# Kernel tuning notes

Measured on AMD Instinct MI355X. Metric: run time of the kernel, lower is better.

Reference implementation:

```python
import jax, jax.numpy as jnp
import numpy as np

N = 100000      # nodes (PF candidates)
E = 1600000     # edges, avg degree 16
CONT = 6        # continuous features
H = 32          # hidden_dim
PDGS = [1, 2, 11, 13, 22, 130, 211]


def _p(k, shape):
    return jax.random.normal(k, shape, jnp.float32) * 0.1


def setup_inputs() -> dict:
    key = jax.random.key(0)
    ks = jax.random.split(key, 24)
    x_cont = jax.random.normal(ks[0], (N, CONT), jnp.float32)
    pdg = jnp.array(PDGS, jnp.int32)[jax.random.randint(ks[1], (N,), 0, 7)]
    sign = jax.random.randint(ks[2], (N,), 0, 2) * 2 - 1
    charge = jax.random.randint(ks[3], (N,), -1, 2)
    pv = jax.random.randint(ks[4], (N,), 0, 8)
    x_cat = jnp.stack([pdg * sign, charge, pv], axis=1).astype(jnp.int32)
    edge_index = jax.random.randint(ks[5], (2, E), 0, N, jnp.int32)
    batch = jnp.zeros((N,), jnp.int32)
    return {
        "x_cont": x_cont, "x_cat": x_cat, "edge_index": edge_index, "batch": batch,
        "W_cont": _p(ks[6], (CONT, H // 2)), "b_cont": jnp.zeros((H // 2,), jnp.float32),
        "T_chrg": _p(ks[7], (3, H // 4)), "T_pdg": _p(ks[8], (7, H // 4)), "T_pv": _p(ks[9], (8, H // 4)),
        "W_cat": _p(ks[10], (3 * H // 4, H // 2)), "b_cat": jnp.zeros((H // 2,), jnp.float32),
        "W_enc": _p(ks[11], (H, H)), "b_enc": jnp.zeros((H,), jnp.float32),
        "g_all": jnp.ones((H,), jnp.float32), "be_all": jnp.zeros((H,), jnp.float32),
        "W_msg": _p(ks[12], (2 * H, H)), "b_msg": jnp.zeros((H,), jnp.float32),
        "g_conv": jnp.ones((H,), jnp.float32), "be_conv": jnp.zeros((H,), jnp.float32),
        "W_out1": _p(ks[13], (H, H // 2)), "b_out1": jnp.zeros((H // 2,), jnp.float32),
        "W_out2": _p(ks[14], (H // 2, 1)), "b_out2": jnp.zeros((1,), jnp.float32),
    }


def _batchnorm(x, gamma, beta, eps=1e-5):
    # training-mode BatchNorm1d: biased batch stats over the node axis
    mu = jnp.mean(x, axis=0)
    var = jnp.mean(jnp.square(x - mu), axis=0)
    return (x - mu) * jax.lax.rsqrt(var + eps) * gamma + beta


def reference(x_cont, x_cat, edge_index, batch,
              W_cont, b_cont, T_chrg, T_pdg, T_pv, W_cat, b_cat,
              W_enc, b_enc, g_all, be_all, W_msg, b_msg, g_conv, be_conv,
              W_out1, b_out1, W_out2, b_out2):
    elu = jax.nn.elu
    emb_cont = elu(x_cont @ W_cont + b_cont)                      # [N, H/2]
    emb_chrg = T_chrg[x_cat[:, 1] + 1]                            # [N, H/4]
    emb_pv = T_pv[x_cat[:, 2]]                                    # [N, H/4]
    pdg_remap = jnp.abs(x_cat[:, 0])
    for i, pdgval in enumerate(PDGS):  # fixed small constant loop, as in original
        pdg_remap = jnp.where(pdg_remap == pdgval, jnp.int32(i), pdg_remap)
    emb_pdg = T_pdg[pdg_remap]                                    # [N, H/4]
    emb_cat = elu(jnp.concatenate([emb_chrg, emb_pdg, emb_pv], axis=1) @ W_cat + b_cat)
    emb = elu(jnp.concatenate([emb_cat, emb_cont], axis=1) @ W_enc + b_enc)
    emb = _batchnorm(emb, g_all, be_all)                          # [N, H]
    # EdgeConv: m_ij = nn([x_i, x_j - x_i]), aggregate by max over incoming edges
    src, dst = edge_index[0], edge_index[1]
    x_i = emb[dst]
    x_j = emb[src]
    msg = jnp.concatenate([x_i, x_j - x_i], axis=1) @ W_msg + b_msg   # [E, H]
    agg = jax.ops.segment_max(msg, dst, num_segments=N)
    agg = jnp.where(jnp.isfinite(agg), agg, 0.0)                  # nodes w/o in-edges -> 0
    emb = emb + _batchnorm(agg, g_conv, be_conv)
    out = elu(emb @ W_out1 + b_out1) @ W_out2 + b_out2            # [N, 1]
    return out.squeeze(-1)
```

## Files before the change

kernel.cpp:

```cpp
#include <hip/hip_runtime.h>
#include <hip/hip_bf16.h>

#define NN 100000
#define EE 1600000
#define NB_SCAN 391

#define NBUCK 782
#define CPAD  16
#define NPART 391
#define NE4   400000
#define CAP   4096
#define CAPSH 12
#define BCAP  2560

typedef __hip_bfloat16 bf16_t;
typedef int int4v __attribute__((ext_vector_type(4)));
typedef float f4 __attribute__((ext_vector_type(4)));

#define PARB  600000
#define EMB   604480
#define PBUF  3804480
#define QBUF  7004480
#define ABUF  10204480
#define SOFF  13404480
#define PART2 (SOFF + 256)
#define CURS  (PART2 + 4096)
#define ROWP2 (CURS + 12512)
#define OFLB  (ROWP2 + 200000)
#define PEB   (OFLB + 3200004)
#define SRCB  (PEB + 3203072)

#define O_WCONT 0
#define O_BCONT 96
#define O_TCHRG 112
#define O_TPDG  136
#define O_TPV   192
#define O_WCAT  256
#define O_BCAT  640
#define O_WENC  656
#define O_BENC  1680
#define O_GALL  1712
#define O_BEALL 1744
#define O_WMSG  1776
#define O_BMSG  3824
#define O_GCONV 3856
#define O_BECONV 3888
#define O_WOUT1 3920
#define O_BOUT1 4432
#define O_WOUT2 4448
#define O_BOUT2 4464
#define NPAR    4465

__device__ __forceinline__ float bf(unsigned short u) {
    return __uint_as_float(((unsigned)u) << 16);
}
__device__ __forceinline__ f4 elu4(f4 v) {
    f4 r;
    r.x = v.x > 0.0f ? v.x : expm1f(v.x);
    r.y = v.y > 0.0f ? v.y : expm1f(v.y);
    r.z = v.z > 0.0f ? v.z : expm1f(v.z);
    r.w = v.w > 0.0f ? v.w : expm1f(v.w);
    return r;
}
__device__ __forceinline__ f4 f4max(f4 a, f4 b) {
    f4 r;
    r.x = fmaxf(a.x, b.x); r.y = fmaxf(a.y, b.y);
    r.z = fmaxf(a.z, b.z); r.w = fmaxf(a.w, b.w);
    return r;
}

struct InitArgs {
    const void* p[19];
    const unsigned short* wdet;
    int*        flagw;
    float*      par;
    int*        curs;
    float*      stats;
    float*      part;
    int*        ofl;
    int*        tcur;
};

__global__ __launch_bounds__(256) void k_init(InitArgs a)
{
    const int offs[20] = {O_WCONT,O_BCONT,O_TCHRG,O_TPDG,O_TPV,O_WCAT,O_BCAT,O_WENC,
                          O_BENC,O_GALL,O_BEALL,O_WMSG,O_BMSG,O_GCONV,O_BECONV,
                          O_WOUT1,O_BOUT1,O_WOUT2,O_BOUT2,NPAR};
    __shared__ int sflag;
    int b = blockIdx.x, tid = threadIdx.x;
    int g = b * 256 + tid;
    if (g < NBUCK) a.curs[g * CPAD] = g << CAPSH;
    if (g < 4096) a.part[g] = 0.0f;
    if (g < 128) a.stats[g] = 0.0f;
    if (g == 0) { a.ofl[0] = 0; *a.tcur = NBUCK << CAPSH; }
    if (b == 0) {
        if (tid == 0) sflag = 0;
        __syncthreads();
        int bad = 0;
        for (int i = tid; i < 1024; i += 256) {
            unsigned e = (a.wdet[i] >> 7) & 0xFFu;
            if (e >= 137u) bad = 1;
        }
        if (bad) atomicOr(&sflag, 1);
        __syncthreads();
        int f32 = sflag;
        if (tid == 0) *a.flagw = f32;
        for (int i = tid; i < NPAR; i += 256) {
            int t = 0;
            while (offs[t + 1] <= i) t++;
            int l = i - offs[t];
            const void* s = a.p[t];
            a.par[i] = f32 ? ((const float*)s)[l] : bf(((const unsigned short*)s)[l]);
        }
    }
}

struct SMemPart {
    int cnt[NBUCK];
    int lstart[NBUCK];
    int gstart[NBUCK];
    int tsum[256];
    unsigned short bkof[4096];
    int staged[4096];
};
struct SMemEmb  { float wc[96], bc[16], tc[24], tp[56], tv[64],
                  wcat[384], bcat[16], we[1024], be[32], ls[64]; };
union SMemA { SMemPart p; SMemEmb e; };

__global__ __launch_bounds__(256, 1) void k_fA(
    const int* __restrict__ eidx, int* __restrict__ curs,
    int* __restrict__ pe, int* __restrict__ ofl, int2* __restrict__ ofl2,
    const void* __restrict__ xc, const int* __restrict__ x_cat,
    const float* __restrict__ par, const int* __restrict__ flag,
    float* __restrict__ emb, float* __restrict__ stats)
{
    __shared__ alignas(16) SMemA sm;
    int tid = threadIdx.x;
    int b = blockIdx.x;

    if (b < NPART) {
        for (int i = tid; i < NBUCK; i += 256) sm.p.cnt[i] = 0;
        __syncthreads();
        const int4v* src4 = (const int4v*)eidx;
        const int4v* dst4 = (const int4v*)(eidx + EE);
        int i0 = b << 10;
        int i1 = i0 + 1024; if (i1 > NE4) i1 = NE4;
        int nE = (i1 - i0) * 4;
        for (int i = i0 + tid; i < i1; i += 256) {
            int4v d = dst4[i];
            atomicAdd(&sm.p.cnt[d.x >> 7], 1);
            atomicAdd(&sm.p.cnt[d.y >> 7], 1);
            atomicAdd(&sm.p.cnt[d.z >> 7], 1);
            atomicAdd(&sm.p.cnt[d.w >> 7], 1);
        }
        __syncthreads();
        int base = tid * 4;
        int c0 = (base     < NBUCK) ? sm.p.cnt[base    ] : 0;
        int c1 = (base + 1 < NBUCK) ? sm.p.cnt[base + 1] : 0;
        int c2 = (base + 2 < NBUCK) ? sm.p.cnt[base + 2] : 0;
        int c3 = (base + 3 < NBUCK) ? sm.p.cnt[base + 3] : 0;
        int s = c0 + c1 + c2 + c3;
        sm.p.tsum[tid] = s;
        __syncthreads();
        for (int off = 1; off < 256; off <<= 1) {
            int x = (tid >= off) ? sm.p.tsum[tid - off] : 0;
            __syncthreads();
            sm.p.tsum[tid] += x;
            __syncthreads();
        }
        int run = sm.p.tsum[tid] - s;
        if (base < NBUCK) {
            sm.p.lstart[base] = run;
            if (c0) sm.p.gstart[base] = atomicAdd(&curs[base * CPAD], c0);
            run += c0;
        }
        if (base + 1 < NBUCK) {
            sm.p.lstart[base + 1] = run;
            if (c1) sm.p.gstart[base + 1] = atomicAdd(&curs[(base + 1) * CPAD], c1);
            run += c1;
        }
        if (base + 2 < NBUCK) {
            sm.p.lstart[base + 2] = run;
            if (c2) sm.p.gstart[base + 2] = atomicAdd(&curs[(base + 2) * CPAD], c2);
            run += c2;
        }
        if (base + 3 < NBUCK) {
            sm.p.lstart[base + 3] = run;
            if (c3) sm.p.gstart[base + 3] = atomicAdd(&curs[(base + 3) * CPAD], c3);
            run += c3;
        }
        __syncthreads();
        for (int i = tid; i < NBUCK; i += 256) {
            int st = sm.p.lstart[i], c = sm.p.cnt[i];
            for (int j = 0; j < c; j++) sm.p.bkof[st + j] = (unsigned short)i;
        }
        __syncthreads();
        for (int i = tid; i < NBUCK; i += 256) sm.p.cnt[i] = 0;
        __syncthreads();
        for (int i = i0 + tid; i < i1; i += 256) {
            int4v s4 = src4[i];
            int4v d4 = dst4[i];
            #define PLACE(SS, DD) { \
                int bk = (DD) >> 7; \
                int r = atomicAdd(&sm.p.cnt[bk], 1); \
                sm.p.staged[sm.p.lstart[bk] + r] = ((SS) << 7) | ((DD) & 127); }
            PLACE(s4.x, d4.x) PLACE(s4.y, d4.y) PLACE(s4.z, d4.z) PLACE(s4.w, d4.w)
            #undef PLACE
        }
        __syncthreads();
        for (int j = tid; j < nE; j += 256) {
            int bk = sm.p.bkof[j];
            int slot = sm.p.gstart[bk] + (j - sm.p.lstart[bk]);
            int packed = sm.p.staged[j];
            if (slot < ((bk + 1) << CAPSH)) pe[slot] = packed;
            else { int oi = atomicAdd(ofl, 1); ofl2[oi] = make_int2(bk, packed); }
        }
        return;
    }

    {
        float* s;
        s=sm.e.wc;   for(int i=tid;i<96;  i+=256) s[i]=par[O_WCONT+i];
        s=sm.e.bc;   for(int i=tid;i<16;  i+=256) s[i]=par[O_BCONT+i];
        s=sm.e.tc;   for(int i=tid;i<24;  i+=256) s[i]=par[O_TCHRG+i];
        s=sm.e.tp;   for(int i=tid;i<56;  i+=256) s[i]=par[O_TPDG+i];
        s=sm.e.tv;   for(int i=tid;i<64;  i+=256) s[i]=par[O_TPV+i];
        s=sm.e.wcat; for(int i=tid;i<384; i+=256) s[i]=par[O_WCAT+i];
        s=sm.e.bcat; for(int i=tid;i<16;  i+=256) s[i]=par[O_BCAT+i];
        s=sm.e.we;   for(int i=tid;i<1024;i+=256) s[i]=par[O_WENC+i];
        s=sm.e.be;   for(int i=tid;i<32;  i+=256) s[i]=par[O_BENC+i];
        if (tid < 64) sm.e.ls[tid] = 0.0f;
    }
    __syncthreads();

    int n = (b - NPART) * 256 + tid;
    float v[64];
    #pragma unroll
    for (int i = 0; i < 64; i++) v[i] = 0.0f;

    if (n < NN) {
        f4* sWc4 = (f4*)sm.e.wc;  f4* sbc4 = (f4*)sm.e.bc;
        f4* sTc4 = (f4*)sm.e.tc;  f4* sTp4 = (f4*)sm.e.tp;  f4* sTv4 = (f4*)sm.e.tv;
        f4* sWcat4 = (f4*)sm.e.wcat; f4* sbcat4 = (f4*)sm.e.bcat;
        f4* sWe4 = (f4*)sm.e.we;  f4* sbe4 = (f4*)sm.e.be;

        float x0,x1,x2,x3,x4,x5;
        if (*flag) {
            const float* xr = (const float*)xc + (size_t)n * 6;
            x0=xr[0]; x1=xr[1]; x2=xr[2]; x3=xr[3]; x4=xr[4]; x5=xr[5];
        } else {
            const unsigned* xr = (const unsigned*)xc + (size_t)n * 3;
            unsigned w0=xr[0], w1=xr[1], w2=xr[2];
            x0=__uint_as_float(w0<<16); x1=__uint_as_float(w0 & 0xFFFF0000u);
            x2=__uint_as_float(w1<<16); x3=__uint_as_float(w1 & 0xFFFF0000u);
            x4=__uint_as_float(w2<<16); x5=__uint_as_float(w2 & 0xFFFF0000u);
        }

        f4 ec[4];
        #pragma unroll
        for (int g = 0; g < 4; g++) {
            f4 acc = sbc4[g];
            acc += x0 * sWc4[0*4+g]; acc += x1 * sWc4[1*4+g]; acc += x2 * sWc4[2*4+g];
            acc += x3 * sWc4[3*4+g]; acc += x4 * sWc4[4*4+g]; acc += x5 * sWc4[5*4+g];
            ec[g] = elu4(acc);
        }

        int c0 = x_cat[n*3+0], c1 = x_cat[n*3+1], c2 = x_cat[n*3+2];
        int a0 = c0 < 0 ? -c0 : c0;
        int pi = (a0==1)?0:(a0==2)?1:(a0==11)?2:(a0==13)?3:(a0==22)?4:(a0==130)?5:6;
        int ci = c1 + 1;

        f4 t0a = sTc4[ci*2],  t0b = sTc4[ci*2+1];
        f4 t1a = sTp4[pi*2],  t1b = sTp4[pi*2+1];
        f4 t2a = sTv4[c2*2],  t2b = sTv4[c2*2+1];

        f4 ecat[4];
        #pragma unroll
        for (int g = 0; g < 4; g++) {
            f4 acc = sbcat4[g];
            #pragma unroll
            for (int k = 0; k < 4; k++) acc += t0a[k] * sWcat4[(k     )*4+g];
            #pragma unroll
            for (int k = 0; k < 4; k++) acc += t0b[k] * sWcat4[(4 + k )*4+g];
            #pragma unroll
            for (int k = 0; k < 4; k++) acc += t1a[k] * sWcat4[(8 + k )*4+g];
            #pragma unroll
            for (int k = 0; k < 4; k++) acc += t1b[k] * sWcat4[(12 + k)*4+g];
            #pragma unroll
            for (int k = 0; k < 4; k++) acc += t2a[k] * sWcat4[(16 + k)*4+g];
            #pragma unroll
            for (int k = 0; k < 4; k++) acc += t2b[k] * sWcat4[(20 + k)*4+g];
            ecat[g] = elu4(acc);
        }

        f4* o = (f4*)(emb + (size_t)n * 32);
        #pragma unroll
        for (int cg = 0; cg < 8; cg++) {
            f4 acc = sbe4[cg];
            #pragma unroll
            for (int kg = 0; kg < 4; kg++) {
                #pragma unroll
                for (int k = 0; k < 4; k++)
                    acc += ecat[kg][k] * sWe4[(kg*4+k)*8 + cg];
            }
            #pragma unroll
            for (int kg = 0; kg < 4; kg++) {
                #pragma unroll
                for (int k = 0; k < 4; k++)
                    acc += ec[kg][k] * sWe4[(16 + kg*4+k)*8 + cg];
            }
            f4 val = elu4(acc);
            o[cg] = val;
            #pragma unroll
            for (int k = 0; k < 4; k++) {
                v[cg*4+k]      = val[k];
                v[32+cg*4+k]   = val[k] * val[k];
            }
        }
    }

    int lane = tid & 63;
    #pragma unroll
    for (int st = 0; st < 6; st++) {
        int off = 1 << st;
        int keep = (lane >> st) & 1;
        int L2 = 32 >> st;
        #pragma unroll
        for (int i = 0; i < 32; i++) {
            if (i < L2) {
                float lo = v[i], hi = v[L2 + i];
                float sent = keep ? lo : hi;
                float got = __shfl_xor(sent, off);
                v[i] = (keep ? hi : lo) + got;
            }
        }
    }
    int idx = ((lane&1)<<5)|((lane&2)<<3)|((lane&4)<<1)|((lane&8)>>1)|((lane&16)>>3)|((lane&32)>>5);
    atomicAdd(&sm.e.ls[idx], v[0]);
    __syncthreads();
    if (tid < 64) atomicAdd(&stats[tid], sm.e.ls[tid]);
}

struct SMemCsr { int stage[BCAP]; int cnt[128]; int sc[128]; int ex[128]; int tl; };
struct SMemPq  { float wp[1024], wq[1024], bp[32], bq[32], ssc[32], ssh[32]; };
union SMemB { SMemCsr c; SMemPq q; };

__global__ __launch_bounds__(256) void k_fB(
    const int* __restrict__ curs, const int* __restrict__ pe,
    const int* __restrict__ ofl, const int2* __restrict__ ofl2,
    int* __restrict__ tcur, int2* __restrict__ rowp2, int* __restrict__ srcl,
    const float* __restrict__ emb, const float* __restrict__ stats,
    const float* __restrict__ par, float* __restrict__ P, float* __restrict__ Q)
{
    __shared__ alignas(16) SMemB sm;
    int tid = threadIdx.x;
    int b = blockIdx.x;

    if (b < NBUCK) {
        int beg = b << CAPSH;
        int m_res = curs[b * CPAD] - beg;
        int stored = m_res < CAP ? m_res : CAP;
        int no = ofl[0];
        if (tid < 128) sm.c.cnt[tid] = 0;
        __syncthreads();
        for (int i = tid; i < stored; i += 256) {
            int p = pe[beg + i];
            if (i < BCAP) sm.c.stage[i] = p;
            atomicAdd(&sm.c.cnt[p & 127], 1);
        }
        for (int j = tid; j < no; j += 256) {
            int2 oe = ofl2[j];
            if (oe.x == b) atomicAdd(&sm.c.cnt[oe.y & 127], 1);
        }
        __syncthreads();
        if (tid < 128) sm.c.sc[tid] = sm.c.cnt[tid];
        __syncthreads();
        for (int off = 1; off < 128; off <<= 1) {
            int x = (tid >= off && tid < 128) ? sm.c.sc[tid - off] : 0;
            __syncthreads();
            if (tid < 128) sm.c.sc[tid] += x;
            __syncthreads();
        }
        int obeg = beg;
        if (m_res > CAP) {
            if (tid == 0) sm.c.tl = atomicAdd(tcur, m_res);
            __syncthreads();
            obeg = sm.c.tl;
        }
        if (tid < 128) {
            int e0 = sm.c.sc[tid] - sm.c.cnt[tid];
            int deg = sm.c.cnt[tid];
            sm.c.ex[tid] = e0;
            int node = b * 128 + tid;
            if (node < NN) rowp2[node] = make_int2(obeg + e0, obeg + e0 + deg);
            sm.c.cnt[tid] = 0;
        }
        __syncthreads();
        for (int i = tid; i < stored; i += 256) {
            int p = (i < BCAP) ? sm.c.stage[i] : pe[beg + i];
            int dl = p & 127;
            int r = atomicAdd(&sm.c.cnt[dl], 1);
            srcl[obeg + sm.c.ex[dl] + r] = p >> 7;
        }
        for (int j = tid; j < no; j += 256) {
            int2 oe = ofl2[j];
            if (oe.x == b) {
                int dl = oe.y & 127;
                int r = atomicAdd(&sm.c.cnt[dl], 1);
                srcl[obeg + sm.c.ex[dl] + r] = oe.y >> 7;
            }
        }
        return;
    }

    if (tid < 32) {
        float mu  = stats[tid] * (1.0f / NN);
        float var = stats[32 + tid] * (1.0f / NN) - mu * mu;
        float s   = par[O_GALL + tid] * rsqrtf(var + 1e-5f);
        sm.q.ssc[tid] = s;
        sm.q.ssh[tid] = par[O_BEALL + tid] - mu * s;
    }
    __syncthreads();
    for (int e = tid; e < 1024; e += 256) {
        int k = e >> 5;
        float w1 = par[O_WMSG + e];
        float w2 = par[O_WMSG + 1024 + e];
        sm.q.wp[e] = sm.q.ssc[k] * (w1 - w2);
        sm.q.wq[e] = sm.q.ssc[k] * w2;
    }
    if (tid < 32) {
        float aP = par[O_BMSG + tid], aQ = 0.0f;
        for (int k = 0; k < 32; k++) {
            float w1 = par[O_WMSG + k*32 + tid];
            float w2 = par[O_WMSG + (k+32)*32 + tid];
            aP += sm.q.ssh[k] * (w1 - w2);
            aQ += sm.q.ssh[k] * w2;
        }
        sm.q.bp[tid] = aP;
        sm.q.bq[tid] = aQ;
    }
    __syncthreads();

    int n = (b - NBUCK) * 256 + tid;
    if (n >= NN) return;

    f4* sWP4 = (f4*)sm.q.wp; f4* sWQ4 = (f4*)sm.q.wq;
    f4* sbP4 = (f4*)sm.q.bp; f4* sbQ4 = (f4*)sm.q.bq;
    const f4* er = (const f4*)(emb + (size_t)n * 32);
    f4 e[8];
    #pragma unroll
    for (int g = 0; g < 8; g++) e[g] = er[g];
    f4* pr = (f4*)(P + (size_t)n * 32);
    f4* qr = (f4*)(Q + (size_t)n * 32);
    #pragma unroll
    for (int cg = 0; cg < 8; cg++) {
        f4 aP = sbP4[cg];
        f4 aQ = sbQ4[cg];
        #pragma unroll
        for (int kg = 0; kg < 8; kg++) {
            #pragma unroll
            for (int k = 0; k < 4; k++) {
                float ek = e[kg][k];
                aP += ek * sWP4[(kg*4+k)*8 + cg];
                aQ += ek * sWQ4[(kg*4+k)*8 + cg];
            }
        }
        pr[cg] = aP;
        qr[cg] = aQ;
    }
}

__global__ __launch_bounds__(256) void k_gather(
    const int2* __restrict__ rowp2, const int* __restrict__ srcl,
    const float* __restrict__ Q, const float* __restrict__ P,
    float* __restrict__ agg, float* __restrict__ part)
{
    __shared__ float ls[64];
    int tid = threadIdx.x;
    if (tid < 64) ls[tid] = 0.0f;
    __syncthreads();

    int lane = tid & 63;
    int wave = tid >> 6;
    int n = blockIdx.x * 4 + wave;
    int slice = lane >> 3;
    int cg    = lane & 7;
    int2 be = rowp2[n];
    int beg = be.x, end = be.y;
    const f4* Q4 = (const f4*)Q;

    f4 pv = (f4){0.f, 0.f, 0.f, 0.f};
    if (lane < 8 && end > beg) pv = ((const f4*)P)[(size_t)n * 8 + lane];

    f4 m = {-INFINITY, -INFINITY, -INFINITY, -INFINITY};
    for (int e = beg + slice; e < end; e += 32) {
        int e1 = min(e + 8,  end - 1);
        int e2 = min(e + 16, end - 1);
        int e3 = min(e + 24, end - 1);
        int s0 = __builtin_nontemporal_load(&srcl[e]);
        int s1 = __builtin_nontemporal_load(&srcl[e1]);
        int s2 = __builtin_nontemporal_load(&srcl[e2]);
        int s3 = __builtin_nontemporal_load(&srcl[e3]);
        f4 q0 = Q4[(size_t)s0 * 8 + cg];
        f4 q1 = Q4[(size_t)s1 * 8 + cg];
        f4 q2 = Q4[(size_t)s2 * 8 + cg];
        f4 q3 = Q4[(size_t)s3 * 8 + cg];
        q0 = f4max(q0, q1);
        q2 = f4max(q2, q3);
        m = f4max(m, f4max(q0, q2));
    }
    #pragma unroll
    for (int off = 8; off < 64; off <<= 1) {
        m.x = fmaxf(m.x, __shfl_xor(m.x, off));
        m.y = fmaxf(m.y, __shfl_xor(m.y, off));
        m.z = fmaxf(m.z, __shfl_xor(m.z, off));
        m.w = fmaxf(m.w, __shfl_xor(m.w, off));
    }
    if (lane < 8) {
        f4 o;
        if (end > beg) o = m + pv;
        else           o = (f4){0.f, 0.f, 0.f, 0.f};
        ((f4*)agg)[(size_t)n * 8 + lane] = o;
        atomicAdd(&ls[cg*4+0], o.x);
        atomicAdd(&ls[cg*4+1], o.y);
        atomicAdd(&ls[cg*4+2], o.z);
        atomicAdd(&ls[cg*4+3], o.w);
        atomicAdd(&ls[32+cg*4+0], o.x*o.x);
        atomicAdd(&ls[32+cg*4+1], o.y*o.y);
        atomicAdd(&ls[32+cg*4+2], o.z*o.z);
        atomicAdd(&ls[32+cg*4+3], o.w*o.w);
    }
    __syncthreads();
    if (tid < 64) atomicAdd(&part[(blockIdx.x & 63) * 64 + tid], ls[tid]);
}

__global__ __launch_bounds__(256, 1) void k_out(
    const float* __restrict__ emb, const float* __restrict__ agg,
    const float* __restrict__ par, const float* __restrict__ stats,
    const float* __restrict__ part,
    const int* __restrict__ flag, void* __restrict__ out)
{
    __shared__ f4 sW14[128];
    __shared__ f4 sb14[4], sW24[4];
    __shared__ f4 sc14[8], sh14[8], sc24[8], sh24[8];
    __shared__ float spart[64];
    __shared__ float sb2s;
    int tid = threadIdx.x;
    {
        float* s = (float*)sW14;
        for (int i = tid; i < 512; i += 256) s[i] = par[O_WOUT1 + i];
    }
    if (tid < 16) {
        ((float*)sb14)[tid] = par[O_BOUT1 + tid];
        ((float*)sW24)[tid] = par[O_WOUT2 + tid];
    }
    if (tid < 64) {
        float acc2 = 0.0f;
        #pragma unroll 8
        for (int r = 0; r < 64; r++) acc2 += part[r * 64 + tid];
        spart[tid] = acc2;
    }
    if (tid == 0) sb2s = par[O_BOUT2];
    __syncthreads();
    if (tid < 32) {
        float mu  = stats[tid] * (1.0f / NN);
        float var = stats[32 + tid] * (1.0f / NN) - mu * mu;
        float s   = par[O_GALL + tid] * rsqrtf(var + 1e-5f);
        ((float*)sc14)[tid] = s;
        ((float*)sh14)[tid] = par[O_BEALL + tid] - mu * s;
        float mu2  = spart[tid] * (1.0f / NN);
        float var2 = spart[32 + tid] * (1.0f / NN) - mu2 * mu2;
        float s2   = par[O_GCONV + tid] * rsqrtf(var2 + 1e-5f);
        ((float*)sc24)[tid] = s2;
        ((float*)sh24)[tid] = par[O_BECONV + tid] - mu2 * s2;
    }
    __syncthreads();

    int n = blockIdx.x * 256 + tid;
    if (n >= NN) return;

    const f4* er = (const f4*)(emb + (size_t)n * 32);
    const f4* ar = (const f4*)(agg + (size_t)n * 32);
    f4 h[8];
    #pragma unroll
    for (int g = 0; g < 8; g++) {
        f4 ev = er[g];
        f4 av = ar[g];
        h[g] = ev * sc14[g] + sh14[g] + av * sc24[g] + sh24[g];
    }
    f4 o1[4];
    #pragma unroll
    for (int g = 0; g < 4; g++) {
        f4 acc = sb14[g];
        #pragma unroll
        for (int kg = 0; kg < 8; kg++) {
            #pragma unroll
            for (int k = 0; k < 4; k++)
                acc += h[kg][k] * sW14[(kg*4+k)*4 + g];
        }
        o1[g] = elu4(acc);
    }
    float acc = sb2s;
    #pragma unroll
    for (int g = 0; g < 4; g++) {
        f4 p = o1[g] * sW24[g];
        acc += p.x + p.y + p.z + p.w;
    }

    if (*flag) ((float*)out)[n] = acc;
    else       ((bf16_t*)out)[n] = __float2bfloat16(acc);
}


extern "C" void kernel_launch(void* const* d_in, const int* in_sizes, int n_in,
                              void* d_out, int out_size, void* d_ws, size_t ws_size,
                              hipStream_t stream)
{
    const void* x_cont = d_in[0];
    const int* x_cat = (const int*)d_in[1];
    const int* eidx  = (const int*)d_in[2];

    float* ws    = (float*)d_ws;
    float* par   = ws + PARB;
    float* emb   = ws + EMB;
    float* P     = ws + PBUF;
    float* Q     = ws + QBUF;
    float* agg   = ws + ABUF;
    float* stats = ws + SOFF;
    int*   flag  = (int*)(stats + 128);
    int*   tcur  = (int*)(stats + 130);
    float* part  = ws + PART2;
    int*   curs  = (int*)(ws + CURS);
    int2*  rowp2 = (int2*)(ws + ROWP2);
    int*   ofl   = (int*)(ws + OFLB);
    int2*  ofl2  = (int2*)(ws + OFLB + 2);
    int*   pe    = (int*)(ws + PEB);
    int*   srcl  = (int*)(ws + SRCB);

    InitArgs ia;
    for (int t = 0; t < 19; t++) ia.p[t] = d_in[4 + t];
    ia.wdet = (const unsigned short*)d_in[11];
    ia.flagw = flag; ia.par = par; ia.curs = curs; ia.stats = stats;
    ia.part = part; ia.ofl = ofl; ia.tcur = tcur;
    k_init<<<16, 256, 0, stream>>>(ia);

    k_fA<<<NPART + NB_SCAN, 256, 0, stream>>>(eidx, curs, pe, ofl, ofl2,
                                              x_cont, x_cat, par, flag, emb, stats);
    k_fB<<<NBUCK + NB_SCAN, 256, 0, stream>>>(curs, pe, ofl, ofl2, tcur, rowp2, srcl,
                                              emb, stats, par, P, Q);
    k_gather<<<NN / 4, 256, 0, stream>>>(rowp2, srcl, Q, P, agg, part);
    k_out<<<NB_SCAN, 256, 0, stream>>>(emb, agg, par, stats, part, flag, d_out);
}
```

Before: 265.6 us.

## Use half-wave per node in gather and move BN stats to separate kernel

k_gather now handles two nodes per wavefront, 32 lanes each. Each iteration covers 16 edges instead of 32, which suits the average in-degree of 16 and keeps fewer lanes idle. The per-block LDS atomic reduction of BatchNorm sums is taken out of the gather and done by a new grid-stride k_stats kernel that writes into stats[64..127]. k_out reads those sums directly instead of summing the 64-row partial buffer. The cost is an extra kernel launch and a second full read of the agg buffer.

```diff
diff --git a/kernel.cpp b/kernel.cpp
--- a/kernel.cpp
+++ b/kernel.cpp
@@ -23,8 +23,7 @@
 #define QBUF  7004480
 #define ABUF  10204480
 #define SOFF  13404480
-#define PART2 (SOFF + 256)
-#define CURS  (PART2 + 4096)
+#define CURS  (SOFF + 256)
 #define ROWP2 (CURS + 12512)
 #define OFLB  (ROWP2 + 200000)
 #define PEB   (OFLB + 3200004)
@@ -76,7 +75,6 @@
     float*      par;
     int*        curs;
     float*      stats;
-    float*      part;
     int*        ofl;
     int*        tcur;
 };
@@ -90,7 +88,6 @@
     int b = blockIdx.x, tid = threadIdx.x;
     int g = b * 256 + tid;
     if (g < NBUCK) a.curs[g * CPAD] = g << CAPSH;
-    if (g < 4096) a.part[g] = 0.0f;
     if (g < 128) a.stats[g] = 0.0f;
     if (g == 0) { a.ofl[0] = 0; *a.tcur = NBUCK << CAPSH; }
     if (b == 0) {
@@ -473,30 +470,28 @@
 __global__ __launch_bounds__(256) void k_gather(
     const int2* __restrict__ rowp2, const int* __restrict__ srcl,
     const float* __restrict__ Q, const float* __restrict__ P,
-    float* __restrict__ agg, float* __restrict__ part)
+    float* __restrict__ agg)
 {
-    __shared__ float ls[64];
     int tid = threadIdx.x;
-    if (tid < 64) ls[tid] = 0.0f;
-    __syncthreads();
-
     int lane = tid & 63;
     int wave = tid >> 6;
-    int n = blockIdx.x * 4 + wave;
-    int slice = lane >> 3;
-    int cg    = lane & 7;
+    int half  = lane >> 5;
+    int hl    = lane & 31;
+    int slice = hl >> 3;
+    int cg    = hl & 7;
+    int n = (blockIdx.x * 4 + wave) * 2 + half;
     int2 be = rowp2[n];
     int beg = be.x, end = be.y;
     const f4* Q4 = (const f4*)Q;
 
     f4 pv = (f4){0.f, 0.f, 0.f, 0.f};
-    if (lane < 8 && end > beg) pv = ((const f4*)P)[(size_t)n * 8 + lane];
+    if (hl < 8 && end > beg) pv = ((const f4*)P)[(size_t)n * 8 + hl];
 
     f4 m = {-INFINITY, -INFINITY, -INFINITY, -INFINITY};
-    for (int e = beg + slice; e < end; e += 32) {
-        int e1 = min(e + 8,  end - 1);
-        int e2 = min(e + 16, end - 1);
-        int e3 = min(e + 24, end - 1);
+    for (int e = beg + slice; e < end; e += 16) {
+        int e1 = min(e + 4,  end - 1);
+        int e2 = min(e + 8,  end - 1);
+        int e3 = min(e + 12, end - 1);
         int s0 = __builtin_nontemporal_load(&srcl[e]);
         int s1 = __builtin_nontemporal_load(&srcl[e1]);
         int s2 = __builtin_nontemporal_load(&srcl[e2]);
@@ -510,40 +505,53 @@
         m = f4max(m, f4max(q0, q2));
     }
     #pragma unroll
-    for (int off = 8; off < 64; off <<= 1) {
+    for (int off = 8; off < 32; off <<= 1) {
         m.x = fmaxf(m.x, __shfl_xor(m.x, off));
         m.y = fmaxf(m.y, __shfl_xor(m.y, off));
         m.z = fmaxf(m.z, __shfl_xor(m.z, off));
         m.w = fmaxf(m.w, __shfl_xor(m.w, off));
     }
-    if (lane < 8) {
+    if (hl < 8) {
         f4 o;
         if (end > beg) o = m + pv;
         else           o = (f4){0.f, 0.f, 0.f, 0.f};
-        ((f4*)agg)[(size_t)n * 8 + lane] = o;
-        atomicAdd(&ls[cg*4+0], o.x);
-        atomicAdd(&ls[cg*4+1], o.y);
-        atomicAdd(&ls[cg*4+2], o.z);
-        atomicAdd(&ls[cg*4+3], o.w);
-        atomicAdd(&ls[32+cg*4+0], o.x*o.x);
-        atomicAdd(&ls[32+cg*4+1], o.y*o.y);
-        atomicAdd(&ls[32+cg*4+2], o.z*o.z);
-        atomicAdd(&ls[32+cg*4+3], o.w*o.w);
-    }
+        ((f4*)agg)[(size_t)n * 8 + hl] = o;
+    }
+}
+
+__global__ __launch_bounds__(256) void k_stats(const float* __restrict__ xin,
+                                               float* __restrict__ outsums, int count)
+{
+    __shared__ float ls[64];
+    int tid = threadIdx.x;
+    if (tid < 64) ls[tid] = 0.0f;
     __syncthreads();
-    if (tid < 64) atomicAdd(&part[(blockIdx.x & 63) * 64 + tid], ls[tid]);
+    int idx = blockIdx.x * 256 + tid;
+    int stride = gridDim.x * 256;
+    int c = idx & 31;
+    float s = 0.0f, q = 0.0f;
+    for (int i = idx; i < count; i += stride) {
+        float v = xin[i];
+        s += v; q += v * v;
+    }
+    s += __shfl_xor(s, 32);
+    q += __shfl_xor(q, 32);
+    if ((tid & 63) < 32) {
+        atomicAdd(&ls[c], s);
+        atomicAdd(&ls[32 + c], q);
+    }
+    __syncthreads();
+    if (tid < 64) atomicAdd(&outsums[tid], ls[tid]);
 }
 
 __global__ __launch_bounds__(256, 1) void k_out(
     const float* __restrict__ emb, const float* __restrict__ agg,
     const float* __restrict__ par, const float* __restrict__ stats,
-    const float* __restrict__ part,
     const int* __restrict__ flag, void* __restrict__ out)
 {
     __shared__ f4 sW14[128];
     __shared__ f4 sb14[4], sW24[4];
     __shared__ f4 sc14[8], sh14[8], sc24[8], sh24[8];
-    __shared__ float spart[64];
     __shared__ float sb2s;
     int tid = threadIdx.x;
     {
@@ -554,26 +562,19 @@
         ((float*)sb14)[tid] = par[O_BOUT1 + tid];
         ((float*)sW24)[tid] = par[O_WOUT2 + tid];
     }
-    if (tid < 64) {
-        float acc2 = 0.0f;
-        #pragma unroll 8
-        for (int r = 0; r < 64; r++) acc2 += part[r * 64 + tid];
-        spart[tid] = acc2;
-    }
-    if (tid == 0) sb2s = par[O_BOUT2];
-    __syncthreads();
     if (tid < 32) {
         float mu  = stats[tid] * (1.0f / NN);
         float var = stats[32 + tid] * (1.0f / NN) - mu * mu;
         float s   = par[O_GALL + tid] * rsqrtf(var + 1e-5f);
         ((float*)sc14)[tid] = s;
         ((float*)sh14)[tid] = par[O_BEALL + tid] - mu * s;
-        float mu2  = spart[tid] * (1.0f / NN);
-        float var2 = spart[32 + tid] * (1.0f / NN) - mu2 * mu2;
+        float mu2  = stats[64 + tid] * (1.0f / NN);
+        float var2 = stats[96 + tid] * (1.0f / NN) - mu2 * mu2;
         float s2   = par[O_GCONV + tid] * rsqrtf(var2 + 1e-5f);
         ((float*)sc24)[tid] = s2;
         ((float*)sh24)[tid] = par[O_BECONV + tid] - mu2 * s2;
     }
+    if (tid == 0) sb2s = par[O_BOUT2];
     __syncthreads();
 
     int n = blockIdx.x * 256 + tid;
@@ -629,7 +630,6 @@
     float* stats = ws + SOFF;
     int*   flag  = (int*)(stats + 128);
     int*   tcur  = (int*)(stats + 130);
-    float* part  = ws + PART2;
     int*   curs  = (int*)(ws + CURS);
     int2*  rowp2 = (int2*)(ws + ROWP2);
     int*   ofl   = (int*)(ws + OFLB);
@@ -641,13 +641,14 @@
     for (int t = 0; t < 19; t++) ia.p[t] = d_in[4 + t];
     ia.wdet = (const unsigned short*)d_in[11];
     ia.flagw = flag; ia.par = par; ia.curs = curs; ia.stats = stats;
-    ia.part = part; ia.ofl = ofl; ia.tcur = tcur;
+    ia.ofl = ofl; ia.tcur = tcur;
     k_init<<<16, 256, 0, stream>>>(ia);
 
     k_fA<<<NPART + NB_SCAN, 256, 0, stream>>>(eidx, curs, pe, ofl, ofl2,
                                               x_cont, x_cat, par, flag, emb, stats);
     k_fB<<<NBUCK + NB_SCAN, 256, 0, stream>>>(curs, pe, ofl, ofl2, tcur, rowp2, srcl,
                                               emb, stats, par, P, Q);
-    k_gather<<<NN / 4, 256, 0, stream>>>(rowp2, srcl, Q, P, agg, part);
-    k_out<<<NB_SCAN, 256, 0, stream>>>(emb, agg, par, stats, part, flag, d_out);
-}
+    k_gather<<<NN / 8, 256, 0, stream>>>(rowp2, srcl, Q, P, agg);
+    k_stats<<<512, 256, 0, stream>>>(agg, stats + 64, NN * 32);
+    k_out<<<NB_SCAN, 256, 0, stream>>>(emb, agg, par, stats, flag, d_out);
+}
```

Result: faster. 255.0 us (-4.0%).
